# Kernel tuning notes

Measured on AMD Instinct MI355X. Metric: run time of the kernel, lower is better.

## Reference

```python
import jax, jax.numpy as jnp
import numpy as np

CAUSAL = True
SOFTMAX_SCALE = 0.125
K_DIFF = 192
MASK_FILL = -1000000.0


def setup_inputs() -> dict:
    key = jax.random.key(0)
    ks = jax.random.split(key, 5)
    shape = (1, 8, 192, 64)  # [batch, n_heads, seq, head_dim]
    return {
        "q": jax.random.normal(ks[0], shape, dtype=jnp.float32),
        "k1": jax.random.normal(ks[1], shape, dtype=jnp.float32),
        "k2": jax.random.normal(ks[2], shape, dtype=jnp.float32),
        "v1": jax.random.normal(ks[3], shape, dtype=jnp.float32),
        "v2": jax.random.normal(ks[4], shape, dtype=jnp.float32),
    }


def reference(q, k1, k2, v1, v2):
    b, n, S, h = q.shape
    # Third-order (trittention) scores.
    score_qk = jnp.einsum("bnth,bnqh->bntq", k2, q)   # [b,n,t,q]
    score_kk = jnp.einsum("bnsh,bnth->bnst", k1, k2)  # [b,n,s,t]
    # score[b,n,s,t,q] = score_kk[b,n,s,t] + score_qk[b,n,t,q]
    score = score_kk[..., None] + score_qk[:, :, None, :, :]
    if CAUSAL:
        # Torch mask (dims named t,s,q over score dims s,t,q):
        # masked where s_score > t_score, t_score > q_score, or t_score - s_score > k_diff
        s_i = jnp.arange(S)[:, None, None]
        t_i = jnp.arange(S)[None, :, None]
        q_i = jnp.arange(S)[None, None, :]
        mask = (s_i > t_i) | (t_i > q_i) | (t_i - s_i > K_DIFF)
        score = jnp.where(mask, MASK_FILL, score)
    pre_softmax_attn_score = score  # [b,n,s,t,q]
    # Rearrange 'b n s t q -> b n q (s t)' and scale.
    flat = jnp.transpose(score, (0, 1, 4, 2, 3)).reshape(b, n, S, S * S) * SOFTMAX_SCALE
    M0 = jnp.max(flat, axis=-1)                       # [b,n,q]
    p = jax.nn.softmax(flat, axis=-1)                  # standard softmax (no +0.01)
    L = jnp.sum(jnp.exp(flat - M0[..., None]), axis=-1) + 0.01
    M = M0 + jnp.log(L)                                # non-standard LSE with +0.01
    # SiLU-gated value combination: v[b,n,s,t,h] = silu(v1[s]) * v2[t]
    v_gated = jax.nn.silu(v1)[:, :, :, None, :] * v2[:, :, None, :, :]
    v_flat = jnp.transpose(v_gated, (0, 1, 4, 2, 3)).reshape(b, n, h, S * S)
    z = jnp.einsum("bnql,bnhl->bnqh", p, v_flat)
    return (z, pre_softmax_attn_score, v_gated, M)
```

## Files before the change

kernel.cpp:

```cpp
#include <hip/hip_runtime.h>
#include <math.h>

#define S 192
#define H 64
#define NH 8
#define SC 0.125f
#define FILLV (-1000000.0f)

__device__ __forceinline__ float wave_max(float v) {
#pragma unroll
  for (int m = 32; m; m >>= 1) v = fmaxf(v, __shfl_xor(v, m));
  return v;
}
__device__ __forceinline__ float wave_sum(float v) {
#pragma unroll
  for (int m = 32; m; m >>= 1) v += __shfl_xor(v, m);
  return v;
}

__global__ __launch_bounds__(256) void k1_kernel(
    const float* __restrict__ q, const float* __restrict__ k1,
    const float* __restrict__ k2, const float* __restrict__ v1,
    float* __restrict__ kk, float* __restrict__ qk, float* __restrict__ qkT,
    float* __restrict__ sv1,
    float* __restrict__ mt, float* __restrict__ St, float* __restrict__ Aw) {
  __shared__ float smem[12996];
  int b = blockIdx.x;
  int tid = threadIdx.x;

  if (b < 864) {
    int p = b / 288, bb = b % 288;
    int n = bb / 36, rem = bb % 36;
    int rt = (rem / 6) * 32, ct = (rem % 6) * 32;
    const float *Abase, *Bbase;
    float* out;
    if (p == 0)      { Abase = k1; Bbase = k2; out = kk; }
    else if (p == 1) { Abase = k2; Bbase = q;  out = qk; }
    else             { Abase = q;  Bbase = k2; out = qkT; }
    Abase += n * S * H; Bbase += n * S * H; out += n * S * S;

    float* As = smem;
    float* Bs = smem + 2080;
    for (int i = tid; i < 32 * 64; i += 256) {
      int r = i >> 6, h = i & 63;
      As[r * 65 + h] = Abase[(rt + r) * H + h];
      Bs[r * 65 + h] = Bbase[(ct + r) * H + h];
    }
    __syncthreads();
    int r0 = (tid / 16) * 2, c0 = (tid % 16) * 2;
    float a00 = 0.f, a01 = 0.f, a10 = 0.f, a11 = 0.f;
#pragma unroll
    for (int h = 0; h < 64; ++h) {
      float x0 = As[r0 * 65 + h], x1 = As[(r0 + 1) * 65 + h];
      float y0 = Bs[c0 * 65 + h], y1 = Bs[(c0 + 1) * 65 + h];
      a00 += x0 * y0; a01 += x0 * y1; a10 += x1 * y0; a11 += x1 * y1;
    }
    out[(rt + r0) * S + ct + c0]         = a00;
    out[(rt + r0) * S + ct + c0 + 1]     = a01;
    out[(rt + r0 + 1) * S + ct + c0]     = a10;
    out[(rt + r0 + 1) * S + ct + c0 + 1] = a11;

  } else if (b < 960) {
    int i = (b - 864) * 256 + tid;
    const float4* v4 = (const float4*)v1;
    float4 x = v4[i];
    float4 y;
    y.x = x.x / (1.f + expf(-x.x));
    y.y = x.y / (1.f + expf(-x.y));
    y.z = x.z / (1.f + expf(-x.z));
    y.w = x.w / (1.f + expf(-x.w));
    ((float4*)sv1)[i] = y;

  } else {
    int idx = b - 960;
    int n = idx / S, t = idx % S;
    int wv = tid >> 6, lane = tid & 63;
    float* k1s  = smem;
    float* k2t  = smem + 12480;
    float* w    = smem + 12544;
    float* red  = smem + 12736;
    float* part = smem + 12740;

    const float* k1b = k1 + n * S * H;
    if (tid < 64) k2t[tid] = k2[(n * S + t) * H + tid];
    int nel = (t + 1) * 64;
    for (int i = tid; i < nel; i += 256) {
      int r = i >> 6, h = i & 63;
      k1s[r * 65 + h] = k1b[i];
    }
    __syncthreads();

    if (tid <= t) {
      float sc = 0.f;
#pragma unroll
      for (int h = 0; h < 64; ++h) sc += k1s[tid * 65 + h] * k2t[h];
      w[tid] = sc;
    }
    __syncthreads();

    float lm = -3.4e38f;
    if (tid <= t) lm = SC * w[tid];
    lm = wave_max(lm);
    if (lane == 0) red[wv] = lm;
    __syncthreads();
    float m = fmaxf(fmaxf(red[0], red[1]), fmaxf(red[2], red[3]));
    __syncthreads();

    float ls = 0.f;
    if (tid <= t) {
      float e = expf(SC * w[tid] - m);
      w[tid] = e;
      ls = e;
    }
    ls = wave_sum(ls);
    if (lane == 0) red[wv] = ls;
    __syncthreads();
    float Ssum = red[0] + red[1] + red[2] + red[3];
    if (tid == 0) { mt[n * S + t] = m; St[n * S + t] = Ssum; }

    const float* v1h = v1 + n * S * H + lane;
    float acc = 0.f;
    for (int s = wv; s <= t; s += 4) {
      float x = v1h[s * H];
      acc += w[s] * (x / (1.f + expf(-x)));
    }
    part[wv * 64 + lane] = acc;
    __syncthreads();
    if (wv == 0)
      Aw[(n * S + t) * H + lane] =
          part[lane] + part[64 + lane] + part[128 + lane] + part[192 + lane];
  }
}

__global__ __launch_bounds__(384) void k2_kernel(
    const float* __restrict__ kk, const float* __restrict__ qk,
    const float* __restrict__ qkT, const float* __restrict__ sv1,
    const float* __restrict__ v2,
    const float* __restrict__ mt, const float* __restrict__ St,
    const float* __restrict__ Aw,
    float* __restrict__ score, float* __restrict__ vg,
    float* __restrict__ z, float* __restrict__ Mout) {
  __shared__ float e[S];
  __shared__ float red[6];
  __shared__ float part[6 * 64];
  int b = blockIdx.x;
  int tid = threadIdx.x;

  if (b < 1536) {
    int n = b / S, s = b % S;
    const float* kkr = kk + (n * S + s) * S;
    const float4* qk4 = (const float4*)(qk + n * S * S);
    float4* out4 = (float4*)(score + (size_t)(n * S + s) * S * S);
    int r = tid / 48;
    int j = tid % 48;
    int q0 = 4 * j;
#pragma unroll 4
    for (int tbase = 0; tbase < S; tbase += 8) {
      int t = tbase + r;
      float kv = kkr[t];
      float4 qv = qk4[t * 48 + j];
      bool rowmask = (t < s);
      float4 v;
      v.x = (rowmask || t > q0)     ? FILLV : kv + qv.x;
      v.y = (rowmask || t > q0 + 1) ? FILLV : kv + qv.y;
      v.z = (rowmask || t > q0 + 2) ? FILLV : kv + qv.z;
      v.w = (rowmask || t > q0 + 3) ? FILLV : kv + qv.w;
      out4[t * 48 + j] = v;
    }

  } else if (b < 3072) {
    int bb = b - 1536;
    int n = bb / S, s = bb % S;
    const float4* a4 = (const float4*)(sv1 + (n * S + s) * H);
    const float4* b4 = (const float4*)(v2 + n * S * H);
    float4* out4 = (float4*)(vg + (size_t)(n * S + s) * S * H);
#pragma unroll
    for (int it = 0; it < 8; ++it) {
      int i = it * 384 + tid;
      int t = i >> 4, j = i & 15;
      float4 a = a4[j];
      float4 bv = b4[t * 16 + j];
      out4[i] = make_float4(a.x * bv.x, a.y * bv.y, a.z * bv.z, a.w * bv.w);
    }

  } else {
    int idx = b - 3072;
    int n = idx / S, qq = idx % S;
    int wv = tid >> 6, lane = tid & 63;
    const float* qkr = qkT + n * S * S + qq * S;
    const float* mtp = mt + n * S;
    const float* Stp = St + n * S;

    float lm = -3.4e38f;
    if (tid <= qq) lm = SC * qkr[tid] + mtp[tid];
    lm = wave_max(lm);
    if (lane == 0) red[wv] = lm;
    __syncthreads();
    float M0 = red[0];
#pragma unroll
    for (int i = 1; i < 6; ++i) M0 = fmaxf(M0, red[i]);
    __syncthreads();

    float ls = 0.f;
    if (tid <= qq) {
      float ev = expf(SC * qkr[tid] + mtp[tid] - M0);
      e[tid] = ev;
      ls = ev * Stp[tid];
    }
    ls = wave_sum(ls);
    if (lane == 0) red[wv] = ls;
    __syncthreads();
    float D = red[0] + red[1] + red[2] + red[3] + red[4] + red[5];
    if (tid == 0) Mout[n * S + qq] = M0 + logf(D + 0.01f);

    const float* vh = v2 + n * S * H + lane;
    const float* Ah = Aw + n * S * H + lane;
    float acc = 0.f;
    for (int t = wv; t <= qq; t += 6) acc += e[t] * vh[t * H] * Ah[t * H];
    part[wv * 64 + lane] = acc;
    __syncthreads();
    if (wv == 0) {
      float zsum = part[lane] + part[64 + lane] + part[128 + lane] +
                   part[192 + lane] + part[256 + lane] + part[320 + lane];
      z[(n * S + qq) * H + lane] = zsum / D;
    }
  }
}

extern "C" void kernel_launch(void* const* d_in, const int* in_sizes, int n_in,
                              void* d_out, int out_size, void* d_ws, size_t ws_size,
                              hipStream_t stream) {
  const float* q  = (const float*)d_in[0];
  const float* k1 = (const float*)d_in[1];
  const float* k2 = (const float*)d_in[2];
  const float* v1 = (const float*)d_in[3];
  const float* v2 = (const float*)d_in[4];
  float* out = (float*)d_out;

  float* z     = out;
  float* score = out + 98304;
  float* vg    = out + 98304 + 56623104;
  float* Mout  = out + 98304 + 56623104 + 18874368;

  float* ws   = (float*)d_ws;
  float* kk   = ws;
  float* qk   = ws + 294912;
  float* qkT  = ws + 589824;
  float* sv1  = ws + 884736;
  float* mt   = ws + 983040;
  float* St   = ws + 984576;
  float* Aw   = ws + 986112;

  k1_kernel<<<dim3(2496), dim3(256), 0, stream>>>(q, k1, k2, v1, kk, qk, qkT,
                                                  sv1, mt, St, Aw);
  k2_kernel<<<dim3(4608), dim3(384), 0, stream>>>(kk, qk, qkT, sv1, v2, mt, St,
                                                  Aw, score, vg, z, Mout);
}
```

Measured before the change: 366.3 us.

## Split fused second kernel into flat elementwise score/vg kernels and output kernel

Splits the multi-role second kernel into three launches: a small z/M output kernel, a flat one-float4-per-thread score writer, and a flat gated-value writer. Each thread now writes one float4 with a fully coalesced linear index instead of looping over rows. This targets better memory-level parallelism and store throughput on the large write-bound outputs. It adds two extra launches and per-thread integer divisions.

```diff
diff --git a/kernel.cpp b/kernel.cpp
--- a/kernel.cpp
+++ b/kernel.cpp
@@ -132,99 +132,93 @@
   }
 }
 
-__global__ __launch_bounds__(384) void k2_kernel(
-    const float* __restrict__ kk, const float* __restrict__ qk,
-    const float* __restrict__ qkT, const float* __restrict__ sv1,
-    const float* __restrict__ v2,
+__global__ __launch_bounds__(384) void out_kernel(
+    const float* __restrict__ qkT, const float* __restrict__ v2,
     const float* __restrict__ mt, const float* __restrict__ St,
     const float* __restrict__ Aw,
-    float* __restrict__ score, float* __restrict__ vg,
     float* __restrict__ z, float* __restrict__ Mout) {
   __shared__ float e[S];
   __shared__ float red[6];
   __shared__ float part[6 * 64];
-  int b = blockIdx.x;
+  int idx = blockIdx.x;
   int tid = threadIdx.x;
-
-  if (b < 1536) {
-    int n = b / S, s = b % S;
-    const float* kkr = kk + (n * S + s) * S;
-    const float4* qk4 = (const float4*)(qk + n * S * S);
-    float4* out4 = (float4*)(score + (size_t)(n * S + s) * S * S);
-    int r = tid / 48;
-    int j = tid % 48;
+  int n = idx / S, qq = idx % S;
+  int wv = tid >> 6, lane = tid & 63;
+  const float* qkr = qkT + n * S * S + qq * S;
+  const float* mtp = mt + n * S;
+  const float* Stp = St + n * S;
+
+  float lm = -3.4e38f;
+  if (tid <= qq) lm = SC * qkr[tid] + mtp[tid];
+  lm = wave_max(lm);
+  if (lane == 0) red[wv] = lm;
+  __syncthreads();
+  float M0 = red[0];
+#pragma unroll
+  for (int i = 1; i < 6; ++i) M0 = fmaxf(M0, red[i]);
+  __syncthreads();
+
+  float ls = 0.f;
+  if (tid <= qq) {
+    float ev = expf(SC * qkr[tid] + mtp[tid] - M0);
+    e[tid] = ev;
+    ls = ev * Stp[tid];
+  }
+  ls = wave_sum(ls);
+  if (lane == 0) red[wv] = ls;
+  __syncthreads();
+  float D = red[0] + red[1] + red[2] + red[3] + red[4] + red[5];
+  if (tid == 0) Mout[n * S + qq] = M0 + logf(D + 0.01f);
+
+  const float* vh = v2 + n * S * H + lane;
+  const float* Ah = Aw + n * S * H + lane;
+  float acc = 0.f;
+  for (int t = wv; t <= qq; t += 6) acc += e[t] * vh[t * H] * Ah[t * H];
+  part[wv * 64 + lane] = acc;
+  __syncthreads();
+  if (wv == 0) {
+    float zsum = part[lane] + part[64 + lane] + part[128 + lane] +
+                 part[192 + lane] + part[256 + lane] + part[320 + lane];
+    z[(n * S + qq) * H + lane] = zsum / D;
+  }
+}
+
+__global__ __launch_bounds__(512) void score_flat(
+    const float* __restrict__ kk, const float* __restrict__ qk,
+    float* __restrict__ score) {
+  int i = blockIdx.x * 512 + threadIdx.x;
+  int j = i % 48;
+  int r = i / 48;
+  int t = r % 192;
+  int ns = r / 192;
+  int s = ns % 192;
+  float4 v;
+  if (t < s) {
+    v = make_float4(FILLV, FILLV, FILLV, FILLV);
+  } else {
+    float kv = kk[ns * 192 + t];
+    float4 qv = ((const float4*)qk)[(ns / 192) * 9216 + t * 48 + j];
     int q0 = 4 * j;
-#pragma unroll 4
-    for (int tbase = 0; tbase < S; tbase += 8) {
-      int t = tbase + r;
-      float kv = kkr[t];
-      float4 qv = qk4[t * 48 + j];
-      bool rowmask = (t < s);
-      float4 v;
-      v.x = (rowmask || t > q0)     ? FILLV : kv + qv.x;
-      v.y = (rowmask || t > q0 + 1) ? FILLV : kv + qv.y;
-      v.z = (rowmask || t > q0 + 2) ? FILLV : kv + qv.z;
-      v.w = (rowmask || t > q0 + 3) ? FILLV : kv + qv.w;
-      out4[t * 48 + j] = v;
-    }
-
-  } else if (b < 3072) {
-    int bb = b - 1536;
-    int n = bb / S, s = bb % S;
-    const float4* a4 = (const float4*)(sv1 + (n * S + s) * H);
-    const float4* b4 = (const float4*)(v2 + n * S * H);
-    float4* out4 = (float4*)(vg + (size_t)(n * S + s) * S * H);
-#pragma unroll
-    for (int it = 0; it < 8; ++it) {
-      int i = it * 384 + tid;
-      int t = i >> 4, j = i & 15;
-      float4 a = a4[j];
-      float4 bv = b4[t * 16 + j];
-      out4[i] = make_float4(a.x * bv.x, a.y * bv.y, a.z * bv.z, a.w * bv.w);
-    }
-
-  } else {
-    int idx = b - 3072;
-    int n = idx / S, qq = idx % S;
-    int wv = tid >> 6, lane = tid & 63;
-    const float* qkr = qkT + n * S * S + qq * S;
-    const float* mtp = mt + n * S;
-    const float* Stp = St + n * S;
-
-    float lm = -3.4e38f;
-    if (tid <= qq) lm = SC * qkr[tid] + mtp[tid];
-    lm = wave_max(lm);
-    if (lane == 0) red[wv] = lm;
-    __syncthreads();
-    float M0 = red[0];
-#pragma unroll
-    for (int i = 1; i < 6; ++i) M0 = fmaxf(M0, red[i]);
-    __syncthreads();
-
-    float ls = 0.f;
-    if (tid <= qq) {
-      float ev = expf(SC * qkr[tid] + mtp[tid] - M0);
-      e[tid] = ev;
-      ls = ev * Stp[tid];
-    }
-    ls = wave_sum(ls);
-    if (lane == 0) red[wv] = ls;
-    __syncthreads();
-    float D = red[0] + red[1] + red[2] + red[3] + red[4] + red[5];
-    if (tid == 0) Mout[n * S + qq] = M0 + logf(D + 0.01f);
-
-    const float* vh = v2 + n * S * H + lane;
-    const float* Ah = Aw + n * S * H + lane;
-    float acc = 0.f;
-    for (int t = wv; t <= qq; t += 6) acc += e[t] * vh[t * H] * Ah[t * H];
-    part[wv * 64 + lane] = acc;
-    __syncthreads();
-    if (wv == 0) {
-      float zsum = part[lane] + part[64 + lane] + part[128 + lane] +
-                   part[192 + lane] + part[256 + lane] + part[320 + lane];
-      z[(n * S + qq) * H + lane] = zsum / D;
-    }
-  }
+    v.x = (t > q0)     ? FILLV : kv + qv.x;
+    v.y = (t > q0 + 1) ? FILLV : kv + qv.y;
+    v.z = (t > q0 + 2) ? FILLV : kv + qv.z;
+    v.w = (t > q0 + 3) ? FILLV : kv + qv.w;
+  }
+  ((float4*)score)[i] = v;
+}
+
+__global__ __launch_bounds__(512) void vg_flat(
+    const float* __restrict__ sv1, const float* __restrict__ v2,
+    float* __restrict__ vg) {
+  int i = blockIdx.x * 512 + threadIdx.x;
+  int j = i % 16;
+  int r = i / 16;
+  int t = r % 192;
+  int ns = r / 192;
+  int n = ns / 192;
+  float4 a = ((const float4*)sv1)[ns * 16 + j];
+  float4 b = ((const float4*)v2)[(n * 192 + t) * 16 + j];
+  ((float4*)vg)[i] = make_float4(a.x * b.x, a.y * b.y, a.z * b.z, a.w * b.w);
 }
 
 extern "C" void kernel_launch(void* const* d_in, const int* in_sizes, int n_in,
@@ -253,6 +247,7 @@
 
   k1_kernel<<<dim3(2496), dim3(256), 0, stream>>>(q, k1, k2, v1, kk, qk, qkT,
                                                   sv1, mt, St, Aw);
-  k2_kernel<<<dim3(4608), dim3(384), 0, stream>>>(kk, qk, qkT, sv1, v2, mt, St,
-                                                  Aw, score, vg, z, Mout);
-}
+  out_kernel<<<dim3(NH * S), dim3(384), 0, stream>>>(qkT, v2, mt, St, Aw, z, Mout);
+  score_flat<<<dim3(27648), dim3(512), 0, stream>>>(kk, qk, score);
+  vg_flat<<<dim3(9216), dim3(512), 0, stream>>>(sv1, v2, vg);
+}
```

Result: no change. 367.6 us (+0.4%).
